# Optimization experiments

Hardware: AMD Instinct MI355X
Metric: run time of the kernel (lower is better)

The kernel has to match this reference:

```python
import jax, jax.numpy as jnp
import numpy as np

N_HEADS = 16
N_KV_HEADS = 4
HEAD_DIM = 128


def apply_rotary_emb(x, cos, sin):
    # x: [B, S, H, D]; cos/sin: [S, D//2]
    xr = x[..., 0::2]
    xi = x[..., 1::2]
    c = cos[None, :, None, :]
    s = sin[None, :, None, :]
    out_r = xr * c - xi * s
    out_i = xr * s + xi * c
    # interleave back: [..., D//2, 2] -> [..., D]
    return jnp.stack([out_r, out_i], axis=-1).reshape(x.shape)


def setup_inputs() -> dict:
    key = jax.random.key(0)
    ks = jax.random.split(key, 7)
    B, S, D = 4, 2048, 2048
    x = jax.random.normal(ks[0], (B, S, D), dtype=jnp.float32)
    # realistic rotary tables
    inv_freq = 1.0 / (10000.0 ** (jnp.arange(0, HEAD_DIM, 2, dtype=jnp.float32) / HEAD_DIM))
    t = jnp.arange(S, dtype=jnp.float32)
    freqs = jnp.outer(t, inv_freq)  # [S, D/2]
    freqs_cos = jnp.cos(freqs)
    freqs_sin = jnp.sin(freqs)
    sc = 0.02
    wq = jax.random.normal(ks[1], (D, N_HEADS * HEAD_DIM), dtype=jnp.float32) * sc
    wk = jax.random.normal(ks[2], (D, N_KV_HEADS * HEAD_DIM), dtype=jnp.float32) * sc
    wv = jax.random.normal(ks[3], (D, N_KV_HEADS * HEAD_DIM), dtype=jnp.float32) * sc
    wo = jax.random.normal(ks[4], (N_HEADS * HEAD_DIM, D), dtype=jnp.float32) * sc
    return {"x": x, "freqs_cos": freqs_cos, "freqs_sin": freqs_sin,
            "wq": wq, "wk": wk, "wv": wv, "wo": wo}


def reference(x, freqs_cos, freqs_sin, wq, wk, wv, wo):
    B, S, D = x.shape
    n_rep = N_HEADS // N_KV_HEADS
    xq = (x @ wq).reshape(B, S, N_HEADS, HEAD_DIM)
    xk = (x @ wk).reshape(B, S, N_KV_HEADS, HEAD_DIM)
    xv = (x @ wv).reshape(B, S, N_KV_HEADS, HEAD_DIM)
    xq = apply_rotary_emb(xq, freqs_cos, freqs_sin)
    xk = apply_rotary_emb(xk, freqs_cos, freqs_sin)
    # repeat_kv (GQA): [B,S,Hkv,D] -> [B,S,Hkv*n_rep,D]
    xk = jnp.repeat(xk, n_rep, axis=2)
    xv = jnp.repeat(xv, n_rep, axis=2)
    # [B,H,S,D]
    q = xq.transpose(0, 2, 1, 3)
    k = xk.transpose(0, 2, 1, 3)
    v = xv.transpose(0, 2, 1, 3)
    scores = jnp.einsum('bhqd,bhkd->bhqk', q, k) / jnp.sqrt(jnp.float32(HEAD_DIM))
    causal = jnp.triu(jnp.ones((S, S), dtype=bool), k=1)
    scores = jnp.where(causal[None, None], -jnp.inf, scores)
    probs = jax.nn.softmax(scores, axis=-1)
    out = jnp.einsum('bhqk,bhkd->bhqd', probs, v)
    out = out.transpose(0, 2, 1, 3).reshape(B, S, N_HEADS * HEAD_DIM)
    return out @ wo
```

## Files before the change

### kernel.cpp

```cpp
#include <hip/hip_runtime.h>
#include <stdint.h>
#include <stddef.h>

#define B_ 4
#define S_ 2048
#define D_ 2048
#define NH 16
#define NKV 4
#define HD 128
#define QKV_N 3072
#define ROWS (B_*S_)

typedef unsigned short u16;
typedef __attribute__((ext_vector_type(8))) unsigned short u16x8;
typedef __attribute__((ext_vector_type(8))) __bf16 bf16x8;
typedef __attribute__((ext_vector_type(4))) float f32x4;

__device__ __forceinline__ u16 f2bf(float f) {
  unsigned u = __builtin_bit_cast(unsigned, f);
  return (u16)((u + 0x7fffu + ((u >> 16) & 1u)) >> 16);
}
__device__ __forceinline__ u16 f2bf_trunc(float f) {
  return (u16)(__builtin_bit_cast(unsigned, f) >> 16);
}
__device__ __forceinline__ float bf2f(u16 h) {
  return __builtin_bit_cast(float, (unsigned)h << 16);
}
__device__ __forceinline__ f32x4 mfma16(u16x8 a, u16x8 b, f32x4 c) {
  return __builtin_amdgcn_mfma_f32_16x16x32_bf16(
      __builtin_bit_cast(bf16x8, a), __builtin_bit_cast(bf16x8, b), c, 0, 0, 0);
}
__device__ __forceinline__ void gld16(const void* g, void* l) {
  __builtin_amdgcn_global_load_lds(
      (const __attribute__((address_space(1))) void*)g,
      (__attribute__((address_space(3))) void*)l, 16, 0, 0);
}

__global__ __launch_bounds__(256) void k_cast_x(const float* __restrict__ x, u16* __restrict__ xb) {
  int i = blockIdx.x * 256 + threadIdx.x;
  float4 v = ((const float4*)x)[i];
  union { u16 u[4]; uint2 p; } o;
  o.u[0] = f2bf(v.x); o.u[1] = f2bf(v.y); o.u[2] = f2bf(v.z); o.u[3] = f2bf(v.w);
  ((uint2*)xb)[i] = o.p;
}

__global__ __launch_bounds__(256) void k_wt(const float* __restrict__ w, u16* __restrict__ wt, int K, int N) {
  __shared__ float tile[32][33];
  int kb = blockIdx.y * 32, nb = blockIdx.x * 32;
  int tx = threadIdx.x, ty = threadIdx.y;
#pragma unroll
  for (int j = 0; j < 32; j += 8)
    tile[ty + j][tx] = w[(size_t)(kb + ty + j) * N + nb + tx];
  __syncthreads();
#pragma unroll
  for (int j = 0; j < 32; j += 8)
    wt[(size_t)(nb + ty + j) * K + kb + tx] = f2bf(tile[tx][ty + j]);
}

template<int NT, bool F32OUT>
__global__ __launch_bounds__(256) void k_gemm(const u16* __restrict__ A, const u16* __restrict__ Bt,
                                              void* __restrict__ C) {
  const int K = 2048;
  __shared__ u16 As[128 * 32];
  __shared__ u16 Bs[128 * 32];
  int mb = blockIdx.y * 128, nb = blockIdx.x * 128;
  int t = threadIdx.x;
  int l = t & 63, lane16 = l & 15, quad = l >> 4;
  int w = t >> 6;
  int wm = (w >> 1) * 64, wn = (w & 1) * 64;
  f32x4 acc[4][4] = {};
  for (int k0 = 0; k0 < K; k0 += 32) {
#pragma unroll
    for (int p = 0; p < 2; ++p) {
      int lin = p * 256 + t;
      int row = lin >> 2, ch = lin & 3;
      gld16(A  + (size_t)(mb + row) * K + k0 + ch * 8, As + (p * 256 + (t & 192)) * 8);
      gld16(Bt + (size_t)(nb + row) * K + k0 + ch * 8, Bs + (p * 256 + (t & 192)) * 8);
    }
    __syncthreads();
    u16x8 af[4], bf[4];
#pragma unroll
    for (int mt = 0; mt < 4; ++mt)
      af[mt] = *(const u16x8*)(As + (wm + mt * 16 + lane16) * 32 + quad * 8);
#pragma unroll
    for (int nt = 0; nt < 4; ++nt)
      bf[nt] = *(const u16x8*)(Bs + (wn + nt * 16 + lane16) * 32 + quad * 8);
#pragma unroll
    for (int mt = 0; mt < 4; ++mt)
#pragma unroll
      for (int nt = 0; nt < 4; ++nt)
        acc[mt][nt] = mfma16(af[mt], bf[nt], acc[mt][nt]);
    __syncthreads();
  }
#pragma unroll
  for (int mt = 0; mt < 4; ++mt)
#pragma unroll
    for (int nt = 0; nt < 4; ++nt)
#pragma unroll
      for (int r = 0; r < 4; ++r) {
        int row = mb + wm + mt * 16 + quad * 4 + r;
        int col = nb + wn + nt * 16 + lane16;
        if constexpr (F32OUT)
          ((float*)C)[(size_t)row * NT + col] = acc[mt][nt][r];
        else
          ((u16*)C)[(size_t)row * NT + col] = f2bf(acc[mt][nt][r]);
      }
}

__global__ __launch_bounds__(256) void k_rope(const u16* __restrict__ qkv, const float* __restrict__ fc,
                                              const float* __restrict__ fs, u16* __restrict__ Q,
                                              u16* __restrict__ Kk) {
  const float SC = 0.1275174214f;
  int row = blockIdx.x;
  int b = row >> 11, s = row & 2047;
  int t = threadIdx.x;
#pragma unroll
  for (int j = 0; j < 5; ++j) {
    int p = t + j * 256;
    int i = p & 63;
    float c = fc[s * 64 + i], sn = fs[s * 64 + i];
    if (p < 1024) {
      int h = p >> 6;
      unsigned pr = *(const unsigned*)(qkv + (size_t)row * QKV_N + h * 128 + 2 * i);
      float xr = bf2f((u16)(pr & 0xffff)), xi = bf2f((u16)(pr >> 16));
      size_t o = (((size_t)(b * NH + h) * S_) + s) * HD + 2 * i;
      unsigned out = (unsigned)f2bf((xr * c - xi * sn) * SC) |
                     ((unsigned)f2bf((xr * sn + xi * c) * SC) << 16);
      *(unsigned*)(Q + o) = out;
    } else {
      int kh = (p - 1024) >> 6;
      unsigned pr = *(const unsigned*)(qkv + (size_t)row * QKV_N + 2048 + kh * 128 + 2 * i);
      float xr = bf2f((u16)(pr & 0xffff)), xi = bf2f((u16)(pr >> 16));
      size_t o = (((size_t)(b * NKV + kh) * S_) + s) * HD + 2 * i;
      unsigned out = (unsigned)f2bf(xr * c - xi * sn) | ((unsigned)f2bf(xr * sn + xi * c) << 16);
      *(unsigned*)(Kk + o) = out;
    }
  }
}

__global__ __launch_bounds__(256) void k_vt(const u16* __restrict__ qkv, u16* __restrict__ Vt) {
  int blk = blockIdx.x;
  int sb = blk & 31, kh = (blk >> 5) & 3, b = blk >> 7;
  int t = threadIdx.x;
  int d = t >> 1, sc = t & 1;
  int s0 = sb * 64 + sc * 32;
  u16 tmp[32];
#pragma unroll
  for (int i = 0; i < 32; ++i)
    tmp[i] = qkv[(size_t)(b * S_ + s0 + i) * QKV_N + 2560 + kh * 128 + d];
  size_t o = ((size_t)(b * NKV + kh) * HD + d) * S_ + s0;
#pragma unroll
  for (int i = 0; i < 32; i += 8)
    *(u16x8*)(Vt + o + i) = *(const u16x8*)(tmp + i);
}

__global__ __launch_bounds__(256) void k_attn(const u16* __restrict__ Q, const u16* __restrict__ Kg,
                                              const u16* __restrict__ Vt, u16* __restrict__ O) {
  int bx = blockIdx.x;
  int bh = bx >> 3, pr = bx & 7;
  int b = bh >> 4, h = bh & 15, kh = h >> 2;
  int t = threadIdx.x;
  int w = t >> 6, l = t & 63, L = l & 15, quad = l >> 4;

  __shared__ u16 Ks[64 * 128];
  __shared__ u16 Vs[144 * 64];
  __shared__ u16 Ps[4][32 * 72];
  u16* Pw = &Ps[w][0];

  const u16* Qh = Q  + ((size_t)(b * NH  + h ) * S_) * HD;
  const u16* Kh = Kg + ((size_t)(b * NKV + kh) * S_) * HD;
  const u16* Vh = Vt + ((size_t)(b * NKV + kh) * HD) * S_;

  if (t < 128) {
    u16x8 ones;
#pragma unroll
    for (int i = 0; i < 8; ++i) ones[i] = 0x3F80;
    *(u16x8*)(Vs + 128 * 64 + t * 8) = ones;
  }

#pragma unroll 1
  for (int half = 0; half < 2; ++half) {
    int qb = half ? (15 - pr) : pr;
    int q0 = qb * 128 + w * 32;

    u16x8 qf[2][4];
#pragma unroll
    for (int m = 0; m < 2; ++m)
#pragma unroll
      for (int kk = 0; kk < 4; ++kk)
        qf[m][kk] = *(const u16x8*)(Qh + (size_t)(q0 + m * 16 + L) * HD + kk * 32 + quad * 8);

    f32x4 acc[2][9] = {};
    int ktiles = 2 * qb + 2;
#pragma unroll 1
    for (int kt = 0; kt < ktiles; ++kt) {
      int kbase = kt * 64;
      __syncthreads();
#pragma unroll
      for (int i = 0; i < 4; ++i) {
        int lin = i * 256 + t;
        int row = lin >> 4, c = lin & 15;
        gld16(Kh + (size_t)(kbase + row) * HD + ((c ^ (row & 7)) * 8),
              Ks + (i * 256 + (t & 192)) * 8);
      }
#pragma unroll
      for (int i = 0; i < 4; ++i) {
        int lin = i * 256 + t;
        int d = lin >> 3, c = lin & 7;
        gld16(Vh + (size_t)d * S_ + kbase + ((c ^ (d & 7)) * 8),
              Vs + (i * 256 + (t & 192)) * 8);
      }
      __syncthreads();
      if (kbase > q0 + 31) continue;

      f32x4 s[2][4] = {};
#pragma unroll
      for (int n = 0; n < 4; ++n)
#pragma unroll
        for (int kk = 0; kk < 4; ++kk) {
          int key = n * 16 + L;
          u16x8 kf = *(const u16x8*)(Ks + key * 128 + (((kk * 4 + quad) ^ (L & 7)) * 8));
          s[0][n] = mfma16(qf[0][kk], kf, s[0][n]);
          s[1][n] = mfma16(qf[1][kk], kf, s[1][n]);
        }
      bool needMask = (kbase + 63 > q0);
#pragma unroll
      for (int m = 0; m < 2; ++m)
#pragma unroll
        for (int n = 0; n < 4; ++n)
#pragma unroll
          for (int r = 0; r < 4; ++r) {
            float e = exp2f(s[m][n][r]);
            if (needMask) {
              int key = kbase + n * 16 + L;
              int qrow = q0 + m * 16 + quad * 4 + r;
              e = (key <= qrow) ? e : 0.0f;
            }
            Pw[(m * 16 + quad * 4 + r) * 72 + n * 16 + L] = f2bf_trunc(e);
          }
#pragma unroll
      for (int kc = 0; kc < 2; ++kc) {
        u16x8 pf0 = *(const u16x8*)(Pw + L * 72 + kc * 32 + quad * 8);
        u16x8 pf1 = *(const u16x8*)(Pw + (16 + L) * 72 + kc * 32 + quad * 8);
#pragma unroll
        for (int nt = 0; nt < 9; ++nt) {
          int d = nt * 16 + L;
          u16x8 vf = *(const u16x8*)(Vs + d * 64 + (((kc * 4 + quad) ^ (L & 7)) * 8));
          acc[0][nt] = mfma16(pf0, vf, acc[0][nt]);
          acc[1][nt] = mfma16(pf1, vf, acc[1][nt]);
        }
      }
    }
#pragma unroll
    for (int m = 0; m < 2; ++m)
#pragma unroll
      for (int r = 0; r < 4; ++r) {
        float inv = 1.0f / acc[m][8][r];
        int qrow = q0 + m * 16 + quad * 4 + r;
#pragma unroll
        for (int nt = 0; nt < 8; ++nt) {
          int col = h * HD + nt * 16 + L;
          O[(size_t)(b * S_ + qrow) * D_ + col] = f2bf(acc[m][nt][r] * inv);
        }
      }
  }
}

extern "C" void kernel_launch(void* const* d_in, const int* in_sizes, int n_in,
                              void* d_out, int out_size, void* d_ws, size_t ws_size,
                              hipStream_t stream) {
  const float* x  = (const float*)d_in[0];
  const float* fc = (const float*)d_in[1];
  const float* fs = (const float*)d_in[2];
  const float* wq = (const float*)d_in[3];
  const float* wk = (const float*)d_in[4];
  const float* wv = (const float*)d_in[5];
  const float* wo = (const float*)d_in[6];
  float* out = (float*)d_out;

  u16* p = (u16*)d_ws;
  u16* xb    = p; p += (size_t)ROWS * D_;
  u16* wqkvT = p; p += (size_t)QKV_N * D_;
  u16* woT   = p; p += (size_t)D_ * D_;
  u16* qkv   = p; p += (size_t)ROWS * QKV_N;
  u16* Qr    = p; p += (size_t)ROWS * (NH * HD);
  u16* Kr    = p; p += (size_t)ROWS * (NKV * HD);
  u16* Vtr   = p; p += (size_t)ROWS * (NKV * HD);
  u16* AO    = p; p += (size_t)ROWS * D_;

  k_cast_x<<<dim3(ROWS * D_ / 1024), dim3(256), 0, stream>>>(x, xb);
  k_wt<<<dim3(64, 64), dim3(32, 8), 0, stream>>>(wq, wqkvT, 2048, 2048);
  k_wt<<<dim3(16, 64), dim3(32, 8), 0, stream>>>(wk, wqkvT + (size_t)2048 * 2048, 2048, 512);
  k_wt<<<dim3(16, 64), dim3(32, 8), 0, stream>>>(wv, wqkvT + (size_t)2560 * 2048, 2048, 512);
  k_wt<<<dim3(64, 64), dim3(32, 8), 0, stream>>>(wo, woT, 2048, 2048);
  k_gemm<QKV_N, false><<<dim3(QKV_N / 128, ROWS / 128), dim3(256), 0, stream>>>(xb, wqkvT, qkv);
  k_rope<<<dim3(ROWS), dim3(256), 0, stream>>>(qkv, fc, fs, Qr, Kr);
  k_vt<<<dim3(B_ * NKV * (S_ / 64)), dim3(256), 0, stream>>>(qkv, Vtr);
  k_attn<<<dim3(64 * 8), dim3(256), 0, stream>>>(Qr, Kr, Vtr, AO);
  k_gemm<D_, true><<<dim3(D_ / 128, ROWS / 128), dim3(256), 0, stream>>>(AO, woT, out);
}
```

Before: 516.9 us.

## Read K/V fragments directly from global memory in attention, dropping LDS staging

The attention kernel no longer stages K and V tiles in shared memory with two barriers per tile. Each lane now loads its MFMA fragments straight from global memory, relying on cache reuse across waves. The ones-rows used for the softmax denominator move into the V-transpose buffer (padded to 144 rows), written by the V-transpose kernel. Each wave also iterates only over the key tiles it needs rather than the block-wide count, removing barrier stalls and idle iterations. The cost is more global/L2 traffic with uncoalesced 16-byte loads and exposed load latency.

```diff
diff --git a/kernel.cpp b/kernel.cpp
--- a/kernel.cpp
+++ b/kernel.cpp
@@ -10,6 +10,7 @@
 #define HD 128
 #define QKV_N 3072
 #define ROWS (B_*S_)
+#define VROWS 144
 
 typedef unsigned short u16;
 typedef __attribute__((ext_vector_type(8))) unsigned short u16x8;
@@ -148,10 +149,18 @@
 #pragma unroll
   for (int i = 0; i < 32; ++i)
     tmp[i] = qkv[(size_t)(b * S_ + s0 + i) * QKV_N + 2560 + kh * 128 + d];
-  size_t o = ((size_t)(b * NKV + kh) * HD + d) * S_ + s0;
+  size_t o = ((size_t)(b * NKV + kh) * VROWS + d) * S_ + s0;
 #pragma unroll
   for (int i = 0; i < 32; i += 8)
     *(u16x8*)(Vt + o + i) = *(const u16x8*)(tmp + i);
+  if (t < 128) {
+    int row = 128 + (t >> 3), c = t & 7;
+    u16x8 ones;
+#pragma unroll
+    for (int i = 0; i < 8; ++i) ones[i] = 0x3F80;
+    size_t o2 = ((size_t)(b * NKV + kh) * VROWS + row) * S_ + sb * 64 + c * 8;
+    *(u16x8*)(Vt + o2) = ones;
+  }
 }
 
 __global__ __launch_bounds__(256) void k_attn(const u16* __restrict__ Q, const u16* __restrict__ Kg,
@@ -162,21 +171,12 @@
   int t = threadIdx.x;
   int w = t >> 6, l = t & 63, L = l & 15, quad = l >> 4;
 
-  __shared__ u16 Ks[64 * 128];
-  __shared__ u16 Vs[144 * 64];
   __shared__ u16 Ps[4][32 * 72];
   u16* Pw = &Ps[w][0];
 
   const u16* Qh = Q  + ((size_t)(b * NH  + h ) * S_) * HD;
   const u16* Kh = Kg + ((size_t)(b * NKV + kh) * S_) * HD;
-  const u16* Vh = Vt + ((size_t)(b * NKV + kh) * HD) * S_;
-
-  if (t < 128) {
-    u16x8 ones;
-#pragma unroll
-    for (int i = 0; i < 8; ++i) ones[i] = 0x3F80;
-    *(u16x8*)(Vs + 128 * 64 + t * 8) = ones;
-  }
+  const u16* Vh = Vt + ((size_t)(b * NKV + kh) * VROWS) * S_;
 
 #pragma unroll 1
   for (int half = 0; half < 2; ++half) {
@@ -191,35 +191,17 @@
         qf[m][kk] = *(const u16x8*)(Qh + (size_t)(q0 + m * 16 + L) * HD + kk * 32 + quad * 8);
 
     f32x4 acc[2][9] = {};
-    int ktiles = 2 * qb + 2;
+    int ktiles = ((q0 + 31) >> 6) + 1;
 #pragma unroll 1
     for (int kt = 0; kt < ktiles; ++kt) {
       int kbase = kt * 64;
-      __syncthreads();
-#pragma unroll
-      for (int i = 0; i < 4; ++i) {
-        int lin = i * 256 + t;
-        int row = lin >> 4, c = lin & 15;
-        gld16(Kh + (size_t)(kbase + row) * HD + ((c ^ (row & 7)) * 8),
-              Ks + (i * 256 + (t & 192)) * 8);
-      }
-#pragma unroll
-      for (int i = 0; i < 4; ++i) {
-        int lin = i * 256 + t;
-        int d = lin >> 3, c = lin & 7;
-        gld16(Vh + (size_t)d * S_ + kbase + ((c ^ (d & 7)) * 8),
-              Vs + (i * 256 + (t & 192)) * 8);
-      }
-      __syncthreads();
-      if (kbase > q0 + 31) continue;
-
+      const u16* kp = Kh + (size_t)(kbase + L) * HD + quad * 8;
       f32x4 s[2][4] = {};
 #pragma unroll
       for (int n = 0; n < 4; ++n)
 #pragma unroll
         for (int kk = 0; kk < 4; ++kk) {
-          int key = n * 16 + L;
-          u16x8 kf = *(const u16x8*)(Ks + key * 128 + (((kk * 4 + quad) ^ (L & 7)) * 8));
+          u16x8 kf = *(const u16x8*)(kp + (size_t)n * 16 * HD + kk * 32);
           s[0][n] = mfma16(qf[0][kk], kf, s[0][n]);
           s[1][n] = mfma16(qf[1][kk], kf, s[1][n]);
         }
@@ -238,14 +220,14 @@
             }
             Pw[(m * 16 + quad * 4 + r) * 72 + n * 16 + L] = f2bf_trunc(e);
           }
+      const u16* vp = Vh + (size_t)L * S_ + kbase + quad * 8;
 #pragma unroll
       for (int kc = 0; kc < 2; ++kc) {
         u16x8 pf0 = *(const u16x8*)(Pw + L * 72 + kc * 32 + quad * 8);
         u16x8 pf1 = *(const u16x8*)(Pw + (16 + L) * 72 + kc * 32 + quad * 8);
 #pragma unroll
         for (int nt = 0; nt < 9; ++nt) {
-          int d = nt * 16 + L;
-          u16x8 vf = *(const u16x8*)(Vs + d * 64 + (((kc * 4 + quad) ^ (L & 7)) * 8));
+          u16x8 vf = *(const u16x8*)(vp + (size_t)nt * 16 * S_ + kc * 32);
           acc[0][nt] = mfma16(pf0, vf, acc[0][nt]);
           acc[1][nt] = mfma16(pf1, vf, acc[1][nt]);
         }
@@ -285,7 +267,7 @@
   u16* qkv   = p; p += (size_t)ROWS * QKV_N;
   u16* Qr    = p; p += (size_t)ROWS * (NH * HD);
   u16* Kr    = p; p += (size_t)ROWS * (NKV * HD);
-  u16* Vtr   = p; p += (size_t)ROWS * (NKV * HD);
+  u16* Vtr   = p; p += (size_t)B_ * NKV * VROWS * S_;
   u16* AO    = p; p += (size_t)ROWS * D_;
 
   k_cast_x<<<dim3(ROWS * D_ / 1024), dim3(256), 0, stream>>>(x, xb);
```

After: 755.9 us. 1.46x slower.

## Double-buffer K/V tiles in attention and transpose V via swizzled LDS

Applied to the files above, without the earlier changes.

The attention kernel now double-buffers the K and V shared-memory tiles and prefetches the next tile while computing the current one. Manual vmcnt waits and raw s_barrier replace the two __syncthreads per iteration. The ones-column in LDS is replaced by a register constant fed to the MFMA, and the P buffer uses an XOR-swizzled 64-wide layout instead of padding. The V-transpose kernel is rewritten to do coalesced vector loads into a swizzled LDS tile and write 16-byte vectors out. The cost is double the LDS footprint, which may lower occupancy, and correctness now depends on the hand-written waitcnt counts.

```diff
diff --git a/kernel.cpp b/kernel.cpp
--- a/kernel.cpp
+++ b/kernel.cpp
@@ -15,6 +15,10 @@
 typedef __attribute__((ext_vector_type(8))) unsigned short u16x8;
 typedef __attribute__((ext_vector_type(8))) __bf16 bf16x8;
 typedef __attribute__((ext_vector_type(4))) float f32x4;
+
+#define WAITVM8() asm volatile("s_waitcnt vmcnt(8)" ::: "memory")
+#define WAITVM0() asm volatile("s_waitcnt vmcnt(0)" ::: "memory")
+#define BAR()     asm volatile("s_barrier" ::: "memory")
 
 __device__ __forceinline__ u16 f2bf(float f) {
   unsigned u = __builtin_bit_cast(unsigned, f);
@@ -139,19 +143,35 @@
 }
 
 __global__ __launch_bounds__(256) void k_vt(const u16* __restrict__ qkv, u16* __restrict__ Vt) {
+  __shared__ u16 tile[64 * 128];
   int blk = blockIdx.x;
   int sb = blk & 31, kh = (blk >> 5) & 3, b = blk >> 7;
   int t = threadIdx.x;
-  int d = t >> 1, sc = t & 1;
-  int s0 = sb * 64 + sc * 32;
-  u16 tmp[32];
-#pragma unroll
-  for (int i = 0; i < 32; ++i)
-    tmp[i] = qkv[(size_t)(b * S_ + s0 + i) * QKV_N + 2560 + kh * 128 + d];
-  size_t o = ((size_t)(b * NKV + kh) * HD + d) * S_ + s0;
-#pragma unroll
-  for (int i = 0; i < 32; i += 8)
-    *(u16x8*)(Vt + o + i) = *(const u16x8*)(tmp + i);
+  int s0 = sb * 64;
+#pragma unroll
+  for (int i = 0; i < 4; ++i) {
+    int lin = i * 256 + t;
+    int row = lin >> 4, c = lin & 15;
+    u16x8 v = *(const u16x8*)(qkv + (size_t)(b * S_ + s0 + row) * QKV_N + 2560 + kh * HD + c * 8);
+    *(u16x8*)(tile + row * 128 + ((c ^ (row & 15)) * 8)) = v;
+  }
+  __syncthreads();
+#pragma unroll
+  for (int i = 0; i < 2; ++i) {
+    int u = i * 256 + t;
+    int p = u >> 3, o = u & 7;
+    u16 lo[8], hi[8];
+#pragma unroll
+    for (int j = 0; j < 8; ++j) {
+      int s = o * 8 + j;
+      int cs = (p >> 2) ^ (s & 15);
+      unsigned v = *(const unsigned*)(tile + s * 128 + cs * 8 + (p & 3) * 2);
+      lo[j] = (u16)(v & 0xffff); hi[j] = (u16)(v >> 16);
+    }
+    size_t ob = ((size_t)(b * NKV + kh) * HD + 2 * p) * S_ + s0 + o * 8;
+    *(u16x8*)(Vt + ob)      = *(u16x8*)lo;
+    *(u16x8*)(Vt + ob + S_) = *(u16x8*)hi;
+  }
 }
 
 __global__ __launch_bounds__(256) void k_attn(const u16* __restrict__ Q, const u16* __restrict__ Kg,
@@ -162,21 +182,18 @@
   int t = threadIdx.x;
   int w = t >> 6, l = t & 63, L = l & 15, quad = l >> 4;
 
-  __shared__ u16 Ks[64 * 128];
-  __shared__ u16 Vs[144 * 64];
-  __shared__ u16 Ps[4][32 * 72];
+  __shared__ u16 Ks[2][64 * 128];
+  __shared__ u16 Vs[2][128 * 64];
+  __shared__ u16 Ps[4][32 * 64];
   u16* Pw = &Ps[w][0];
 
   const u16* Qh = Q  + ((size_t)(b * NH  + h ) * S_) * HD;
   const u16* Kh = Kg + ((size_t)(b * NKV + kh) * S_) * HD;
   const u16* Vh = Vt + ((size_t)(b * NKV + kh) * HD) * S_;
 
-  if (t < 128) {
-    u16x8 ones;
-#pragma unroll
-    for (int i = 0; i < 8; ++i) ones[i] = 0x3F80;
-    *(u16x8*)(Vs + 128 * 64 + t * 8) = ones;
-  }
+  u16x8 ones;
+#pragma unroll
+  for (int i = 0; i < 8; ++i) ones[i] = 0x3F80;
 
 #pragma unroll 1
   for (int half = 0; half < 2; ++half) {
@@ -192,64 +209,89 @@
 
     f32x4 acc[2][9] = {};
     int ktiles = 2 * qb + 2;
+
+    {
+#pragma unroll
+      for (int i = 0; i < 4; ++i) {
+        int lin = i * 256 + t, row = lin >> 4, c = lin & 15;
+        gld16(Kh + (size_t)row * HD + ((c ^ (row & 7)) * 8), &Ks[0][0] + (i * 256 + (t & 192)) * 8);
+      }
+#pragma unroll
+      for (int i = 0; i < 4; ++i) {
+        int lin = i * 256 + t, d = lin >> 3, c = lin & 7;
+        gld16(Vh + (size_t)d * S_ + ((c ^ (d & 7)) * 8), &Vs[0][0] + (i * 256 + (t & 192)) * 8);
+      }
+    }
+
 #pragma unroll 1
     for (int kt = 0; kt < ktiles; ++kt) {
       int kbase = kt * 64;
-      __syncthreads();
-#pragma unroll
-      for (int i = 0; i < 4; ++i) {
-        int lin = i * 256 + t;
-        int row = lin >> 4, c = lin & 15;
-        gld16(Kh + (size_t)(kbase + row) * HD + ((c ^ (row & 7)) * 8),
-              Ks + (i * 256 + (t & 192)) * 8);
-      }
-#pragma unroll
-      for (int i = 0; i < 4; ++i) {
-        int lin = i * 256 + t;
-        int d = lin >> 3, c = lin & 7;
-        gld16(Vh + (size_t)d * S_ + kbase + ((c ^ (d & 7)) * 8),
-              Vs + (i * 256 + (t & 192)) * 8);
-      }
-      __syncthreads();
-      if (kbase > q0 + 31) continue;
-
-      f32x4 s[2][4] = {};
-#pragma unroll
-      for (int n = 0; n < 4; ++n)
-#pragma unroll
-        for (int kk = 0; kk < 4; ++kk) {
-          int key = n * 16 + L;
-          u16x8 kf = *(const u16x8*)(Ks + key * 128 + (((kk * 4 + quad) ^ (L & 7)) * 8));
-          s[0][n] = mfma16(qf[0][kk], kf, s[0][n]);
-          s[1][n] = mfma16(qf[1][kk], kf, s[1][n]);
+      int cur = kt & 1;
+      if (kt + 1 < ktiles) {
+        int nb = kbase + 64;
+#pragma unroll
+        for (int i = 0; i < 4; ++i) {
+          int lin = i * 256 + t, row = lin >> 4, c = lin & 15;
+          gld16(Kh + (size_t)(nb + row) * HD + ((c ^ (row & 7)) * 8),
+                &Ks[cur ^ 1][0] + (i * 256 + (t & 192)) * 8);
         }
-      bool needMask = (kbase + 63 > q0);
-#pragma unroll
-      for (int m = 0; m < 2; ++m)
+#pragma unroll
+        for (int i = 0; i < 4; ++i) {
+          int lin = i * 256 + t, d = lin >> 3, c = lin & 7;
+          gld16(Vh + (size_t)d * S_ + nb + ((c ^ (d & 7)) * 8),
+                &Vs[cur ^ 1][0] + (i * 256 + (t & 192)) * 8);
+        }
+        WAITVM8();
+      } else {
+        WAITVM0();
+      }
+      BAR();
+      if (kbase <= q0 + 31) {
+        const u16* Kst = &Ks[cur][0];
+        const u16* Vst = &Vs[cur][0];
+        f32x4 s[2][4] = {};
 #pragma unroll
         for (int n = 0; n < 4; ++n)
 #pragma unroll
-          for (int r = 0; r < 4; ++r) {
-            float e = exp2f(s[m][n][r]);
-            if (needMask) {
-              int key = kbase + n * 16 + L;
-              int qrow = q0 + m * 16 + quad * 4 + r;
-              e = (key <= qrow) ? e : 0.0f;
+          for (int kk = 0; kk < 4; ++kk) {
+            int key = n * 16 + L;
+            u16x8 kf = *(const u16x8*)(Kst + key * 128 + (((kk * 4 + quad) ^ (L & 7)) * 8));
+            s[0][n] = mfma16(qf[0][kk], kf, s[0][n]);
+            s[1][n] = mfma16(qf[1][kk], kf, s[1][n]);
+          }
+        bool needMask = (kbase + 63 > q0);
+#pragma unroll
+        for (int m = 0; m < 2; ++m)
+#pragma unroll
+          for (int n = 0; n < 4; ++n)
+#pragma unroll
+            for (int r = 0; r < 4; ++r) {
+              float e = exp2f(s[m][n][r]);
+              if (needMask) {
+                int key = kbase + n * 16 + L;
+                int qrow = q0 + m * 16 + quad * 4 + r;
+                e = (key <= qrow) ? e : 0.0f;
+              }
+              int prow = m * 16 + quad * 4 + r;
+              int chunk = n * 2 + (L >> 3);
+              Pw[prow * 64 + ((chunk ^ (prow & 7)) * 8) + (L & 7)] = f2bf_trunc(e);
             }
-            Pw[(m * 16 + quad * 4 + r) * 72 + n * 16 + L] = f2bf_trunc(e);
+#pragma unroll
+        for (int kc = 0; kc < 2; ++kc) {
+          u16x8 pf0 = *(const u16x8*)(Pw + L * 64 + (((kc * 4 + quad) ^ (L & 7)) * 8));
+          u16x8 pf1 = *(const u16x8*)(Pw + (16 + L) * 64 + (((kc * 4 + quad) ^ (L & 7)) * 8));
+#pragma unroll
+          for (int nt = 0; nt < 8; ++nt) {
+            int d = nt * 16 + L;
+            u16x8 vf = *(const u16x8*)(Vst + d * 64 + (((kc * 4 + quad) ^ (L & 7)) * 8));
+            acc[0][nt] = mfma16(pf0, vf, acc[0][nt]);
+            acc[1][nt] = mfma16(pf1, vf, acc[1][nt]);
           }
-#pragma unroll
-      for (int kc = 0; kc < 2; ++kc) {
-        u16x8 pf0 = *(const u16x8*)(Pw + L * 72 + kc * 32 + quad * 8);
-        u16x8 pf1 = *(const u16x8*)(Pw + (16 + L) * 72 + kc * 32 + quad * 8);
-#pragma unroll
-        for (int nt = 0; nt < 9; ++nt) {
-          int d = nt * 16 + L;
-          u16x8 vf = *(const u16x8*)(Vs + d * 64 + (((kc * 4 + quad) ^ (L & 7)) * 8));
-          acc[0][nt] = mfma16(pf0, vf, acc[0][nt]);
-          acc[1][nt] = mfma16(pf1, vf, acc[1][nt]);
+          acc[0][8] = mfma16(pf0, ones, acc[0][8]);
+          acc[1][8] = mfma16(pf1, ones, acc[1][8]);
         }
       }
+      BAR();
     }
 #pragma unroll
     for (int m = 0; m < 2; ++m)
```

After: 566.2 us. 1.1x slower.

## Transpose S via operand swap, pack P writes, tile V transpose through LDS

Applied to the files above, without the earlier changes.

The QK^T MFMA now takes K as the A operand and Q as B, so each lane holds four consecutive keys for one query row. Those four probabilities are packed into bf16 pairs with perm and written to LDS as one 8-byte store instead of scattered 2-byte stores. The row-sum ones column moves from LDS into a register operand, which shrinks the Vs buffer, and LDS/global offsets are precomputed outside the loop. The V transpose kernel now stages a tile through swizzled LDS so both its global reads and writes are vectorized, where it previously did strided scalar loads.

```diff
diff --git a/kernel.cpp b/kernel.cpp
--- a/kernel.cpp
+++ b/kernel.cpp
@@ -19,9 +19,6 @@
 __device__ __forceinline__ u16 f2bf(float f) {
   unsigned u = __builtin_bit_cast(unsigned, f);
   return (u16)((u + 0x7fffu + ((u >> 16) & 1u)) >> 16);
-}
-__device__ __forceinline__ u16 f2bf_trunc(float f) {
-  return (u16)(__builtin_bit_cast(unsigned, f) >> 16);
 }
 __device__ __forceinline__ float bf2f(u16 h) {
   return __builtin_bit_cast(float, (unsigned)h << 16);
@@ -139,19 +136,35 @@
 }
 
 __global__ __launch_bounds__(256) void k_vt(const u16* __restrict__ qkv, u16* __restrict__ Vt) {
+  __shared__ u16 tile[64 * 128];
   int blk = blockIdx.x;
   int sb = blk & 31, kh = (blk >> 5) & 3, b = blk >> 7;
   int t = threadIdx.x;
-  int d = t >> 1, sc = t & 1;
-  int s0 = sb * 64 + sc * 32;
-  u16 tmp[32];
-#pragma unroll
-  for (int i = 0; i < 32; ++i)
-    tmp[i] = qkv[(size_t)(b * S_ + s0 + i) * QKV_N + 2560 + kh * 128 + d];
-  size_t o = ((size_t)(b * NKV + kh) * HD + d) * S_ + s0;
-#pragma unroll
-  for (int i = 0; i < 32; i += 8)
-    *(u16x8*)(Vt + o + i) = *(const u16x8*)(tmp + i);
+  int s0 = sb * 64;
+#pragma unroll
+  for (int i = 0; i < 4; ++i) {
+    int lin = i * 256 + t;
+    int row = lin >> 4, c = lin & 15;
+    u16x8 v = *(const u16x8*)(qkv + (size_t)(b * S_ + s0 + row) * QKV_N + 2560 + kh * HD + c * 8);
+    *(u16x8*)(tile + row * 128 + ((c ^ (row & 15)) * 8)) = v;
+  }
+  __syncthreads();
+#pragma unroll
+  for (int i = 0; i < 2; ++i) {
+    int u = i * 256 + t;
+    int p = u >> 3, o = u & 7;
+    u16 lo[8], hi[8];
+#pragma unroll
+    for (int j = 0; j < 8; ++j) {
+      int s = o * 8 + j;
+      int cs = (p >> 2) ^ (s & 15);
+      unsigned v = *(const unsigned*)(tile + s * 128 + cs * 8 + (p & 3) * 2);
+      lo[j] = (u16)(v & 0xffff); hi[j] = (u16)(v >> 16);
+    }
+    size_t ob = ((size_t)(b * NKV + kh) * HD + 2 * p) * S_ + s0 + o * 8;
+    *(u16x8*)(Vt + ob)      = *(u16x8*)lo;
+    *(u16x8*)(Vt + ob + S_) = *(u16x8*)hi;
+  }
 }
 
 __global__ __launch_bounds__(256) void k_attn(const u16* __restrict__ Q, const u16* __restrict__ Kg,
@@ -163,7 +176,7 @@
   int w = t >> 6, l = t & 63, L = l & 15, quad = l >> 4;
 
   __shared__ u16 Ks[64 * 128];
-  __shared__ u16 Vs[144 * 64];
+  __shared__ u16 Vs[128 * 64];
   __shared__ u16 Ps[4][32 * 72];
   u16* Pw = &Ps[w][0];
 
@@ -171,11 +184,28 @@
   const u16* Kh = Kg + ((size_t)(b * NKV + kh) * S_) * HD;
   const u16* Vh = Vt + ((size_t)(b * NKV + kh) * HD) * S_;
 
-  if (t < 128) {
-    u16x8 ones;
-#pragma unroll
-    for (int i = 0; i < 8; ++i) ones[i] = 0x3F80;
-    *(u16x8*)(Vs + 128 * 64 + t * 8) = ones;
+  u16x8 ones;
+#pragma unroll
+  for (int i = 0; i < 8; ++i) ones[i] = 0x3F80;
+
+  int koff[4], voff[2];
+#pragma unroll
+  for (int kk = 0; kk < 4; ++kk) koff[kk] = 128 * L + 8 * ((4 * kk + quad) ^ (L & 7));
+#pragma unroll
+  for (int kc = 0; kc < 2; ++kc) voff[kc] = 64 * L + 8 * ((4 * kc + quad) ^ (L & 7));
+  const int pread  = 72 * L + 8 * quad;
+  const int pwrite = 72 * L + 4 * quad;
+
+  int kgo[4], vgo[4], klo[4], vlo[4];
+#pragma unroll
+  for (int i = 0; i < 4; ++i) {
+    int lin = i * 256 + t;
+    int row = lin >> 4, c = lin & 15;
+    kgo[i] = row * HD + ((c ^ (row & 7)) * 8);
+    int d = lin >> 3, c2 = lin & 7;
+    vgo[i] = d * S_ + ((c2 ^ (d & 7)) * 8);
+    klo[i] = (i * 256 + (t & 192)) * 8;
+    vlo[i] = (i * 256 + (t & 192)) * 8;
   }
 
 #pragma unroll 1
@@ -196,59 +226,57 @@
     for (int kt = 0; kt < ktiles; ++kt) {
       int kbase = kt * 64;
       __syncthreads();
-#pragma unroll
-      for (int i = 0; i < 4; ++i) {
-        int lin = i * 256 + t;
-        int row = lin >> 4, c = lin & 15;
-        gld16(Kh + (size_t)(kbase + row) * HD + ((c ^ (row & 7)) * 8),
-              Ks + (i * 256 + (t & 192)) * 8);
-      }
-#pragma unroll
-      for (int i = 0; i < 4; ++i) {
-        int lin = i * 256 + t;
-        int d = lin >> 3, c = lin & 7;
-        gld16(Vh + (size_t)d * S_ + kbase + ((c ^ (d & 7)) * 8),
-              Vs + (i * 256 + (t & 192)) * 8);
-      }
+      const u16* Kt = Kh + (size_t)kbase * HD;
+      const u16* Vg = Vh + kbase;
+#pragma unroll
+      for (int i = 0; i < 4; ++i) gld16(Kt + kgo[i], Ks + klo[i]);
+#pragma unroll
+      for (int i = 0; i < 4; ++i) gld16(Vg + vgo[i], Vs + vlo[i]);
       __syncthreads();
       if (kbase > q0 + 31) continue;
 
-      f32x4 s[2][4] = {};
-#pragma unroll
-      for (int n = 0; n < 4; ++n)
+      bool needMask = (kbase + 63 > q0);
+#pragma unroll
+      for (int n = 0; n < 4; ++n) {
+        f32x4 s0v = {}, s1v = {};
 #pragma unroll
         for (int kk = 0; kk < 4; ++kk) {
-          int key = n * 16 + L;
-          u16x8 kf = *(const u16x8*)(Ks + key * 128 + (((kk * 4 + quad) ^ (L & 7)) * 8));
-          s[0][n] = mfma16(qf[0][kk], kf, s[0][n]);
-          s[1][n] = mfma16(qf[1][kk], kf, s[1][n]);
+          u16x8 kf = *(const u16x8*)(Ks + koff[kk] + 2048 * n);
+          s0v = mfma16(kf, qf[0][kk], s0v);
+          s1v = mfma16(kf, qf[1][kk], s1v);
         }
-      bool needMask = (kbase + 63 > q0);
-#pragma unroll
-      for (int m = 0; m < 2; ++m)
-#pragma unroll
-        for (int n = 0; n < 4; ++n)
+#pragma unroll
+        for (int m = 0; m < 2; ++m) {
+          f32x4 sv = m ? s1v : s0v;
+          int qrow = q0 + m * 16 + L;
+          unsigned eu[4];
 #pragma unroll
           for (int r = 0; r < 4; ++r) {
-            float e = exp2f(s[m][n][r]);
+            float e = exp2f(sv[r]);
             if (needMask) {
-              int key = kbase + n * 16 + L;
-              int qrow = q0 + m * 16 + quad * 4 + r;
+              int key = kbase + n * 16 + quad * 4 + r;
               e = (key <= qrow) ? e : 0.0f;
             }
-            Pw[(m * 16 + quad * 4 + r) * 72 + n * 16 + L] = f2bf_trunc(e);
+            eu[r] = __builtin_bit_cast(unsigned, e);
           }
+          uint2 pk;
+          pk.x = __builtin_amdgcn_perm(eu[1], eu[0], 0x07060302u);
+          pk.y = __builtin_amdgcn_perm(eu[3], eu[2], 0x07060302u);
+          *(uint2*)(Pw + pwrite + 1152 * m + 16 * n) = pk;
+        }
+      }
 #pragma unroll
       for (int kc = 0; kc < 2; ++kc) {
-        u16x8 pf0 = *(const u16x8*)(Pw + L * 72 + kc * 32 + quad * 8);
-        u16x8 pf1 = *(const u16x8*)(Pw + (16 + L) * 72 + kc * 32 + quad * 8);
-#pragma unroll
-        for (int nt = 0; nt < 9; ++nt) {
-          int d = nt * 16 + L;
-          u16x8 vf = *(const u16x8*)(Vs + d * 64 + (((kc * 4 + quad) ^ (L & 7)) * 8));
+        u16x8 pf0 = *(const u16x8*)(Pw + pread + 32 * kc);
+        u16x8 pf1 = *(const u16x8*)(Pw + pread + 1152 + 32 * kc);
+#pragma unroll
+        for (int nt = 0; nt < 8; ++nt) {
+          u16x8 vf = *(const u16x8*)(Vs + voff[kc] + 1024 * nt);
           acc[0][nt] = mfma16(pf0, vf, acc[0][nt]);
           acc[1][nt] = mfma16(pf1, vf, acc[1][nt]);
         }
+        acc[0][8] = mfma16(pf0, ones, acc[0][8]);
+        acc[1][8] = mfma16(pf1, ones, acc[1][8]);
       }
     }
 #pragma unroll
```

Result: faster. 500.8 us (-3.1%).
